# Performance work log

Measured on AMD Instinct MI355X. Metric: run time of the kernel, lower is better.

The kernel has to match this reference:

```python
import jax, jax.numpy as jnp
import numpy as np

TEMPERATURE = 8.0  # sqrt(d_k) with d_k = 64
NEG_INF = -jnp.inf


def setup_inputs() -> dict:
    key = jax.random.key(0)
    kq, kk, kv = jax.random.split(key, 3)
    b, n, d = 16, 2048, 64
    q = jax.random.normal(kq, (b, n, d), dtype=jnp.float32)
    k = jax.random.normal(kk, (b, n, d), dtype=jnp.float32)
    v = jax.random.normal(kv, (b, n, d), dtype=jnp.float32)
    # causal mask: True where attention is disallowed (strict upper triangle)
    mask = jnp.broadcast_to(jnp.triu(jnp.ones((n, n), dtype=bool), k=1), (b, n, n))
    return {"q": q, "k": k, "v": v, "mask": mask}


def reference(q, k, v, mask):
    # attn = q @ k^T / temperature   [b, n, n]
    attn = jnp.einsum('bqd,bkd->bqk', q, k) / TEMPERATURE
    attn = jnp.where(mask, NEG_INF, attn)
    attn = jax.nn.softmax(attn, axis=2)
    # output = attn @ v   [b, n, d]
    output = jnp.einsum('bqk,bkd->bqd', attn, v)
    return (output, attn)
```

## Files before the change

kernel.cpp:

```cpp
#include <hip/hip_runtime.h>


constexpr int B = 16;
constexpr int N = 2048;
constexpr int D = 64;
constexpr float INV_TEMP = 0.125f;

typedef __attribute__((ext_vector_type(8))) short bf16x8;
typedef __attribute__((ext_vector_type(4))) float f32x4;

__device__ __forceinline__ short f2bf(float f) {
    __bf16 h = (__bf16)f;
    return __builtin_bit_cast(short, h);
}

__global__ __launch_bounds__(512) void sdpa_flash(
    const float* __restrict__ q,
    const float* __restrict__ k,
    const float* __restrict__ v,
    float* __restrict__ out,
    float* __restrict__ invws)
{
    __shared__ __align__(16) short sK[64][72];
    __shared__ __align__(16) short sV[64][72];
    __shared__ __align__(16) short sPt[32][72];
    __shared__ float rsum[128];
    __shared__ float sinv[32];

    const int x = blockIdx.x;
    const int b = x >> 6;
    const int u = x & 63;
    const int rt = 63 - u;
    const int qs = rt * 32;
    const int ntiles = (rt >> 1) + 1;

    const int t    = threadIdx.x;
    const int w    = t >> 6;
    const int lane = t & 63;
    const int l15  = lane & 15;
    const int quad = lane >> 4;
    const int q8   = quad * 8;
    const int rg   = w & 1;
    const int cg   = w >> 1;

    const float* qb = q + (size_t)b * N * D;
    const float* kb = k + (size_t)b * N * D;
    const float* vb = v + (size_t)b * N * D;

    const int krow = t >> 3;
    const int kc8  = (t & 7) * 8;

    float4 kf0, kf1;
    float  vr[8];

    {
        const float4* s = (const float4*)(kb + (size_t)krow * D + kc8);
        kf0 = s[0]; kf1 = s[1];
        const float* sv = vb + (size_t)(w * 8) * D + lane;
#pragma unroll
        for (int i = 0; i < 8; ++i) vr[i] = sv[(size_t)i * D];
    }

    if (t < 256) {
        const float4* s = (const float4*)(qb + (size_t)(qs + krow) * D + kc8);
        float4 a = s[0], c4 = s[1];
        float qv[8] = {a.x,a.y,a.z,a.w, c4.x,c4.y,c4.z,c4.w};
        bf16x8 pq;
#pragma unroll
        for (int i = 0; i < 8; ++i) pq[i] = f2bf(qv[i]);
        *(bf16x8*)&sK[krow][kc8] = pq;
    }
    __syncthreads();
    const bf16x8 qa0 = *(const bf16x8*)&sK[rg * 16 + l15][q8];
    const bf16x8 qa1 = *(const bf16x8*)&sK[rg * 16 + l15][32 + q8];

    float rs[4] = {0.f, 0.f, 0.f, 0.f};
    f32x4 o = {0.f, 0.f, 0.f, 0.f};

    for (int kt = 0; kt < ntiles; ++kt) {
        __syncthreads();
        {
            float kv[8] = {kf0.x,kf0.y,kf0.z,kf0.w, kf1.x,kf1.y,kf1.z,kf1.w};
            bf16x8 pk, pv;
#pragma unroll
            for (int i = 0; i < 8; ++i) pk[i] = f2bf(kv[i]);
#pragma unroll
            for (int i = 0; i < 8; ++i) pv[i] = f2bf(vr[i]);
            *(bf16x8*)&sK[krow][kc8]  = pk;
            *(bf16x8*)&sV[lane][w*8]  = pv;
        }
        __syncthreads();
        if (kt + 1 < ntiles) {
            const float4* s = (const float4*)(kb + (size_t)((kt+1)*64 + krow) * D + kc8);
            kf0 = s[0]; kf1 = s[1];
            const float* sv = vb + (size_t)((kt+1)*64 + w*8) * D + lane;
#pragma unroll
            for (int i = 0; i < 8; ++i) vr[i] = sv[(size_t)i * D];
        }
        bf16x8 b0 = *(const bf16x8*)&sK[cg * 16 + l15][q8];
        bf16x8 b1 = *(const bf16x8*)&sK[cg * 16 + l15][32 + q8];
        f32x4 c = {0.f, 0.f, 0.f, 0.f};
        c = __builtin_amdgcn_mfma_f32_16x16x32_bf16(qa0, b0, c, 0, 0, 0);
        c = __builtin_amdgcn_mfma_f32_16x16x32_bf16(qa1, b1, c, 0, 0, 0);
        const int colg = kt * 64 + cg * 16 + l15;
#pragma unroll
        for (int r = 0; r < 4; ++r) {
            const int rowg = qs + rg * 16 + quad * 4 + r;
            float pr = (colg <= rowg) ? __expf(c[r] * INV_TEMP) : 0.f;
            rs[r] += pr;
            sPt[rg * 16 + quad * 4 + r][cg * 16 + l15] = f2bf(pr);
        }
        __syncthreads();
#pragma unroll
        for (int kc = 0; kc < 2; ++kc) {
            bf16x8 a  = *(const bf16x8*)&sPt[rg * 16 + l15][kc * 32 + q8];
            bf16x8 vf = *(const bf16x8*)&sV[cg * 16 + l15][kc * 32 + q8];
            o = __builtin_amdgcn_mfma_f32_16x16x32_bf16(a, vf, o, 0, 0, 0);
        }
    }

#pragma unroll
    for (int r = 0; r < 4; ++r) {
        float s = rs[r];
        s += __shfl_xor(s, 1);
        s += __shfl_xor(s, 2);
        s += __shfl_xor(s, 4);
        s += __shfl_xor(s, 8);
        rs[r] = s;
    }
    if (l15 == 0) {
#pragma unroll
        for (int r = 0; r < 4; ++r) rsum[w * 16 + quad * 4 + r] = rs[r];
    }
    __syncthreads();
    if (t < 32) {
        const int rg2 = t >> 4, rl = t & 15;
        float tot = rsum[(rg2 + 0) * 16 + rl] + rsum[(rg2 + 2) * 16 + rl]
                  + rsum[(rg2 + 4) * 16 + rl] + rsum[(rg2 + 6) * 16 + rl];
        sinv[t] = 1.f / tot;
        invws[(size_t)b * N + qs + t] = sinv[t];
    }
    __syncthreads();

#pragma unroll
    for (int r = 0; r < 4; ++r) {
        const int rowl = rg * 16 + quad * 4 + r;
        out[(size_t)(b * N + qs + rowl) * D + cg * 16 + l15] = o[r] * sinv[rowl];
    }
}

__global__ __launch_bounds__(512) void sdpa_attn(
    const float* __restrict__ q,
    const float* __restrict__ k,
    const float* __restrict__ attn_unused,
    float* __restrict__ attn,
    const float* __restrict__ invws)
{
    __shared__ __align__(16) short sQ[32][72];
    __shared__ float sinv[32];

    const int x = blockIdx.x;
    const int b = x >> 6;
    const int u = x & 63;
    const int rt = 63 - u;
    const int qs = rt * 32;
    const int ntiles = (rt >> 1) + 1;

    const int t    = threadIdx.x;
    const int w    = t >> 6;
    const int lane = t & 63;
    const int l15  = lane & 15;
    const int quad = lane >> 4;
    const int q8   = quad * 8;
    const int rg   = w & 1;
    const int cg   = w >> 1;

    const float* qb = q + (size_t)b * N * D;
    const float* kb = k + (size_t)b * N * D;
    float* attn_b = attn + (size_t)b * N * N;

    if (t < 256) {
        const int krow = t >> 3, kc8 = (t & 7) * 8;
        const float4* s = (const float4*)(qb + (size_t)(qs + krow) * D + kc8);
        float4 a = s[0], c4 = s[1];
        float qv[8] = {a.x,a.y,a.z,a.w, c4.x,c4.y,c4.z,c4.w};
        bf16x8 pq;
#pragma unroll
        for (int i = 0; i < 8; ++i) pq[i] = f2bf(qv[i]);
        *(bf16x8*)&sQ[krow][kc8] = pq;
    }
    if (t >= 256 && t < 288) sinv[t - 256] = invws[(size_t)b * N + qs + (t - 256)];
    __syncthreads();

    const bf16x8 qa0 = *(const bf16x8*)&sQ[rg * 16 + l15][q8];
    const bf16x8 qa1 = *(const bf16x8*)&sQ[rg * 16 + l15][32 + q8];

    const int qrow = qs + rg * 16 + l15;
    const float einv = sinv[rg * 16 + l15];
    float* arow = attn_b + (size_t)qrow * N;

    for (int kt = 0; kt < ntiles; ++kt) {
        const float* kr = kb + (size_t)(kt * 64 + cg * 16 + l15) * D;
        const float4* kp = (const float4*)(kr + q8);
        float4 k0 = kp[0], k1 = kp[1];
        const float4* kp2 = (const float4*)(kr + 32 + q8);
        float4 k2 = kp2[0], k3 = kp2[1];
        float kv[16] = {k0.x,k0.y,k0.z,k0.w, k1.x,k1.y,k1.z,k1.w,
                        k2.x,k2.y,k2.z,k2.w, k3.x,k3.y,k3.z,k3.w};
        bf16x8 kb0, kb1;
#pragma unroll
        for (int i = 0; i < 8; ++i) { kb0[i] = f2bf(kv[i]); kb1[i] = f2bf(kv[8 + i]); }

        f32x4 c = {0.f, 0.f, 0.f, 0.f};
        c = __builtin_amdgcn_mfma_f32_16x16x32_bf16(kb0, qa0, c, 0, 0, 0);
        c = __builtin_amdgcn_mfma_f32_16x16x32_bf16(kb1, qa1, c, 0, 0, 0);

        const int kg0 = kt * 64 + cg * 16 + quad * 4;
        float4 pv;
        pv.x = (kg0 + 0 <= qrow) ? __expf(c[0] * INV_TEMP) * einv : 0.f;
        pv.y = (kg0 + 1 <= qrow) ? __expf(c[1] * INV_TEMP) * einv : 0.f;
        pv.z = (kg0 + 2 <= qrow) ? __expf(c[2] * INV_TEMP) * einv : 0.f;
        pv.w = (kg0 + 3 <= qrow) ? __expf(c[3] * INV_TEMP) * einv : 0.f;
        *(float4*)(arow + kg0) = pv;
    }

    const int lim  = ntiles * 64;
    const int erow = t >> 4;
    const int ec   = (t & 15) * 4;
    float* zrow = attn_b + (size_t)(qs + erow) * N;
    const float4 z = {0.f, 0.f, 0.f, 0.f};
    for (int c0 = lim + ec; c0 < N; c0 += 64) {
        *(float4*)(zrow + c0) = z;
    }
}

extern "C" void kernel_launch(void* const* d_in, const int* in_sizes, int n_in,
                              void* d_out, int out_size, void* d_ws, size_t ws_size,
                              hipStream_t stream) {
    const float* q = (const float*)d_in[0];
    const float* k = (const float*)d_in[1];
    const float* v = (const float*)d_in[2];

    float* out  = (float*)d_out;
    float* attn = out + (size_t)B * N * D;
    float* invws = (float*)d_ws;

    sdpa_flash<<<dim3(B * 64), dim3(512), 0, stream>>>(q, k, v, out, invws);
    sdpa_attn <<<dim3(B * 64), dim3(512), 0, stream>>>(q, k, attn, attn, invws);
}
```

Before: 536.2 us.

## Fuse flash and attn-write kernels into one with paired causal row tiles

Merges the two kernels into one launch where each block handles two query row tiles, one long and one short, to balance the causal triangle's work. The normalizer stays in shared memory instead of round-tripping through a workspace buffer, and blocks are mapped so each XCD serves two batches for L2 locality. K/V shared tiles are double-buffered to drop one barrier per iteration, and K loads in the attn-write loop are prefetched one tile ahead. The grid shrinks to 512 blocks, so there is less parallelism and less latency hiding per CU.

```diff
diff --git a/kernel.cpp b/kernel.cpp
--- a/kernel.cpp
+++ b/kernel.cpp
@@ -14,25 +14,24 @@
     return __builtin_bit_cast(short, h);
 }
 
-__global__ __launch_bounds__(512) void sdpa_flash(
+__global__ __launch_bounds__(512) void sdpa_fused2(
     const float* __restrict__ q,
     const float* __restrict__ k,
     const float* __restrict__ v,
     float* __restrict__ out,
-    float* __restrict__ invws)
+    float* __restrict__ attn)
 {
-    __shared__ __align__(16) short sK[64][72];
-    __shared__ __align__(16) short sV[64][72];
+    __shared__ __align__(16) short sK[2][64][72];
+    __shared__ __align__(16) short sV[2][64][72];
     __shared__ __align__(16) short sPt[32][72];
     __shared__ float rsum[128];
     __shared__ float sinv[32];
 
-    const int x = blockIdx.x;
-    const int b = x >> 6;
-    const int u = x & 63;
-    const int rt = 63 - u;
-    const int qs = rt * 32;
-    const int ntiles = (rt >> 1) + 1;
+    const int x   = blockIdx.x;
+    const int xcd = x & 7;
+    const int idx = x >> 3;
+    const int b   = xcd * 2 + (idx & 1);
+    const int u   = idx >> 1;
 
     const int t    = threadIdx.x;
     const int w    = t >> 6;
@@ -46,191 +45,159 @@
     const float* qb = q + (size_t)b * N * D;
     const float* kb = k + (size_t)b * N * D;
     const float* vb = v + (size_t)b * N * D;
+    float* attn_b = attn + (size_t)b * N * N;
 
     const int krow = t >> 3;
     const int kc8  = (t & 7) * 8;
 
-    float4 kf0, kf1;
-    float  vr[8];
-
-    {
-        const float4* s = (const float4*)(kb + (size_t)krow * D + kc8);
-        kf0 = s[0]; kf1 = s[1];
-        const float* sv = vb + (size_t)(w * 8) * D + lane;
-#pragma unroll
-        for (int i = 0; i < 8; ++i) vr[i] = sv[(size_t)i * D];
-    }
-
-    if (t < 256) {
-        const float4* s = (const float4*)(qb + (size_t)(qs + krow) * D + kc8);
-        float4 a = s[0], c4 = s[1];
-        float qv[8] = {a.x,a.y,a.z,a.w, c4.x,c4.y,c4.z,c4.w};
-        bf16x8 pq;
-#pragma unroll
-        for (int i = 0; i < 8; ++i) pq[i] = f2bf(qv[i]);
-        *(bf16x8*)&sK[krow][kc8] = pq;
-    }
-    __syncthreads();
-    const bf16x8 qa0 = *(const bf16x8*)&sK[rg * 16 + l15][q8];
-    const bf16x8 qa1 = *(const bf16x8*)&sK[rg * 16 + l15][32 + q8];
-
-    float rs[4] = {0.f, 0.f, 0.f, 0.f};
-    f32x4 o = {0.f, 0.f, 0.f, 0.f};
-
-    for (int kt = 0; kt < ntiles; ++kt) {
-        __syncthreads();
+    for (int h = 0; h < 2; ++h) {
+        const int rt = h ? u : (63 - u);
+        const int qs = rt * 32;
+        const int nt = (rt >> 1) + 1;
+
+        float4 kf0, kf1;
+        float  vr[8];
         {
-            float kv[8] = {kf0.x,kf0.y,kf0.z,kf0.w, kf1.x,kf1.y,kf1.z,kf1.w};
-            bf16x8 pk, pv;
-#pragma unroll
-            for (int i = 0; i < 8; ++i) pk[i] = f2bf(kv[i]);
-#pragma unroll
-            for (int i = 0; i < 8; ++i) pv[i] = f2bf(vr[i]);
-            *(bf16x8*)&sK[krow][kc8]  = pk;
-            *(bf16x8*)&sV[lane][w*8]  = pv;
-        }
-        __syncthreads();
-        if (kt + 1 < ntiles) {
-            const float4* s = (const float4*)(kb + (size_t)((kt+1)*64 + krow) * D + kc8);
+            const float4* s = (const float4*)(kb + (size_t)krow * D + kc8);
             kf0 = s[0]; kf1 = s[1];
-            const float* sv = vb + (size_t)((kt+1)*64 + w*8) * D + lane;
+            const float* sv = vb + (size_t)(w * 8) * D + lane;
 #pragma unroll
             for (int i = 0; i < 8; ++i) vr[i] = sv[(size_t)i * D];
         }
-        bf16x8 b0 = *(const bf16x8*)&sK[cg * 16 + l15][q8];
-        bf16x8 b1 = *(const bf16x8*)&sK[cg * 16 + l15][32 + q8];
-        f32x4 c = {0.f, 0.f, 0.f, 0.f};
-        c = __builtin_amdgcn_mfma_f32_16x16x32_bf16(qa0, b0, c, 0, 0, 0);
-        c = __builtin_amdgcn_mfma_f32_16x16x32_bf16(qa1, b1, c, 0, 0, 0);
-        const int colg = kt * 64 + cg * 16 + l15;
+
+        __syncthreads();
+        if (t < 256) {
+            const float4* s = (const float4*)(qb + (size_t)(qs + krow) * D + kc8);
+            float4 a = s[0], c4 = s[1];
+            float qv[8] = {a.x,a.y,a.z,a.w, c4.x,c4.y,c4.z,c4.w};
+            bf16x8 pq;
+#pragma unroll
+            for (int i = 0; i < 8; ++i) pq[i] = f2bf(qv[i]);
+            *(bf16x8*)&sPt[krow][kc8] = pq;
+        }
+        __syncthreads();
+        const bf16x8 qa0 = *(const bf16x8*)&sPt[rg * 16 + l15][q8];
+        const bf16x8 qa1 = *(const bf16x8*)&sPt[rg * 16 + l15][32 + q8];
+
+        float rs[4] = {0.f, 0.f, 0.f, 0.f};
+        f32x4 o = {0.f, 0.f, 0.f, 0.f};
+
+        for (int kt = 0; kt < nt; ++kt) {
+            const int cur = kt & 1;
+            {
+                float kv[8] = {kf0.x,kf0.y,kf0.z,kf0.w, kf1.x,kf1.y,kf1.z,kf1.w};
+                bf16x8 pk, pv;
+#pragma unroll
+                for (int i = 0; i < 8; ++i) pk[i] = f2bf(kv[i]);
+#pragma unroll
+                for (int i = 0; i < 8; ++i) pv[i] = f2bf(vr[i]);
+                *(bf16x8*)&sK[cur][krow][kc8]  = pk;
+                *(bf16x8*)&sV[cur][lane][w*8]  = pv;
+            }
+            __syncthreads();
+            if (kt + 1 < nt) {
+                const float4* s = (const float4*)(kb + (size_t)((kt+1)*64 + krow) * D + kc8);
+                kf0 = s[0]; kf1 = s[1];
+                const float* sv = vb + (size_t)((kt+1)*64 + w*8) * D + lane;
+#pragma unroll
+                for (int i = 0; i < 8; ++i) vr[i] = sv[(size_t)i * D];
+            }
+            bf16x8 b0 = *(const bf16x8*)&sK[cur][cg * 16 + l15][q8];
+            bf16x8 b1 = *(const bf16x8*)&sK[cur][cg * 16 + l15][32 + q8];
+            f32x4 c = {0.f, 0.f, 0.f, 0.f};
+            c = __builtin_amdgcn_mfma_f32_16x16x32_bf16(qa0, b0, c, 0, 0, 0);
+            c = __builtin_amdgcn_mfma_f32_16x16x32_bf16(qa1, b1, c, 0, 0, 0);
+            const int colg = kt * 64 + cg * 16 + l15;
+#pragma unroll
+            for (int r = 0; r < 4; ++r) {
+                const int rowg = qs + rg * 16 + quad * 4 + r;
+                float pr = (colg <= rowg) ? __expf(c[r] * INV_TEMP) : 0.f;
+                rs[r] += pr;
+                sPt[rg * 16 + quad * 4 + r][cg * 16 + l15] = f2bf(pr);
+            }
+            __syncthreads();
+#pragma unroll
+            for (int kc = 0; kc < 2; ++kc) {
+                bf16x8 a  = *(const bf16x8*)&sPt[rg * 16 + l15][kc * 32 + q8];
+                bf16x8 vf = *(const bf16x8*)&sV[cur][cg * 16 + l15][kc * 32 + q8];
+                o = __builtin_amdgcn_mfma_f32_16x16x32_bf16(a, vf, o, 0, 0, 0);
+            }
+        }
+
 #pragma unroll
         for (int r = 0; r < 4; ++r) {
-            const int rowg = qs + rg * 16 + quad * 4 + r;
-            float pr = (colg <= rowg) ? __expf(c[r] * INV_TEMP) : 0.f;
-            rs[r] += pr;
-            sPt[rg * 16 + quad * 4 + r][cg * 16 + l15] = f2bf(pr);
-        }
-        __syncthreads();
-#pragma unroll
-        for (int kc = 0; kc < 2; ++kc) {
-            bf16x8 a  = *(const bf16x8*)&sPt[rg * 16 + l15][kc * 32 + q8];
-            bf16x8 vf = *(const bf16x8*)&sV[cg * 16 + l15][kc * 32 + q8];
-            o = __builtin_amdgcn_mfma_f32_16x16x32_bf16(a, vf, o, 0, 0, 0);
-        }
-    }
-
-#pragma unroll
-    for (int r = 0; r < 4; ++r) {
-        float s = rs[r];
-        s += __shfl_xor(s, 1);
-        s += __shfl_xor(s, 2);
-        s += __shfl_xor(s, 4);
-        s += __shfl_xor(s, 8);
-        rs[r] = s;
-    }
-    if (l15 == 0) {
-#pragma unroll
-        for (int r = 0; r < 4; ++r) rsum[w * 16 + quad * 4 + r] = rs[r];
-    }
-    __syncthreads();
-    if (t < 32) {
-        const int rg2 = t >> 4, rl = t & 15;
-        float tot = rsum[(rg2 + 0) * 16 + rl] + rsum[(rg2 + 2) * 16 + rl]
-                  + rsum[(rg2 + 4) * 16 + rl] + rsum[(rg2 + 6) * 16 + rl];
-        sinv[t] = 1.f / tot;
-        invws[(size_t)b * N + qs + t] = sinv[t];
-    }
-    __syncthreads();
-
-#pragma unroll
-    for (int r = 0; r < 4; ++r) {
-        const int rowl = rg * 16 + quad * 4 + r;
-        out[(size_t)(b * N + qs + rowl) * D + cg * 16 + l15] = o[r] * sinv[rowl];
-    }
-}
-
-__global__ __launch_bounds__(512) void sdpa_attn(
-    const float* __restrict__ q,
-    const float* __restrict__ k,
-    const float* __restrict__ attn_unused,
-    float* __restrict__ attn,
-    const float* __restrict__ invws)
-{
-    __shared__ __align__(16) short sQ[32][72];
-    __shared__ float sinv[32];
-
-    const int x = blockIdx.x;
-    const int b = x >> 6;
-    const int u = x & 63;
-    const int rt = 63 - u;
-    const int qs = rt * 32;
-    const int ntiles = (rt >> 1) + 1;
-
-    const int t    = threadIdx.x;
-    const int w    = t >> 6;
-    const int lane = t & 63;
-    const int l15  = lane & 15;
-    const int quad = lane >> 4;
-    const int q8   = quad * 8;
-    const int rg   = w & 1;
-    const int cg   = w >> 1;
-
-    const float* qb = q + (size_t)b * N * D;
-    const float* kb = k + (size_t)b * N * D;
-    float* attn_b = attn + (size_t)b * N * N;
-
-    if (t < 256) {
-        const int krow = t >> 3, kc8 = (t & 7) * 8;
-        const float4* s = (const float4*)(qb + (size_t)(qs + krow) * D + kc8);
-        float4 a = s[0], c4 = s[1];
-        float qv[8] = {a.x,a.y,a.z,a.w, c4.x,c4.y,c4.z,c4.w};
-        bf16x8 pq;
-#pragma unroll
-        for (int i = 0; i < 8; ++i) pq[i] = f2bf(qv[i]);
-        *(bf16x8*)&sQ[krow][kc8] = pq;
-    }
-    if (t >= 256 && t < 288) sinv[t - 256] = invws[(size_t)b * N + qs + (t - 256)];
-    __syncthreads();
-
-    const bf16x8 qa0 = *(const bf16x8*)&sQ[rg * 16 + l15][q8];
-    const bf16x8 qa1 = *(const bf16x8*)&sQ[rg * 16 + l15][32 + q8];
-
-    const int qrow = qs + rg * 16 + l15;
-    const float einv = sinv[rg * 16 + l15];
-    float* arow = attn_b + (size_t)qrow * N;
-
-    for (int kt = 0; kt < ntiles; ++kt) {
-        const float* kr = kb + (size_t)(kt * 64 + cg * 16 + l15) * D;
-        const float4* kp = (const float4*)(kr + q8);
-        float4 k0 = kp[0], k1 = kp[1];
-        const float4* kp2 = (const float4*)(kr + 32 + q8);
-        float4 k2 = kp2[0], k3 = kp2[1];
-        float kv[16] = {k0.x,k0.y,k0.z,k0.w, k1.x,k1.y,k1.z,k1.w,
-                        k2.x,k2.y,k2.z,k2.w, k3.x,k3.y,k3.z,k3.w};
-        bf16x8 kb0, kb1;
-#pragma unroll
-        for (int i = 0; i < 8; ++i) { kb0[i] = f2bf(kv[i]); kb1[i] = f2bf(kv[8 + i]); }
-
-        f32x4 c = {0.f, 0.f, 0.f, 0.f};
-        c = __builtin_amdgcn_mfma_f32_16x16x32_bf16(kb0, qa0, c, 0, 0, 0);
-        c = __builtin_amdgcn_mfma_f32_16x16x32_bf16(kb1, qa1, c, 0, 0, 0);
-
-        const int kg0 = kt * 64 + cg * 16 + quad * 4;
-        float4 pv;
-        pv.x = (kg0 + 0 <= qrow) ? __expf(c[0] * INV_TEMP) * einv : 0.f;
-        pv.y = (kg0 + 1 <= qrow) ? __expf(c[1] * INV_TEMP) * einv : 0.f;
-        pv.z = (kg0 + 2 <= qrow) ? __expf(c[2] * INV_TEMP) * einv : 0.f;
-        pv.w = (kg0 + 3 <= qrow) ? __expf(c[3] * INV_TEMP) * einv : 0.f;
-        *(float4*)(arow + kg0) = pv;
-    }
-
-    const int lim  = ntiles * 64;
-    const int erow = t >> 4;
-    const int ec   = (t & 15) * 4;
-    float* zrow = attn_b + (size_t)(qs + erow) * N;
-    const float4 z = {0.f, 0.f, 0.f, 0.f};
-    for (int c0 = lim + ec; c0 < N; c0 += 64) {
-        *(float4*)(zrow + c0) = z;
+            float s = rs[r];
+            s += __shfl_xor(s, 1);
+            s += __shfl_xor(s, 2);
+            s += __shfl_xor(s, 4);
+            s += __shfl_xor(s, 8);
+            rs[r] = s;
+        }
+        if (l15 == 0) {
+#pragma unroll
+            for (int r = 0; r < 4; ++r) rsum[w * 16 + quad * 4 + r] = rs[r];
+        }
+        __syncthreads();
+        if (t < 32) {
+            const int rg2 = t >> 4, rl = t & 15;
+            float tot = rsum[(rg2 + 0) * 16 + rl] + rsum[(rg2 + 2) * 16 + rl]
+                      + rsum[(rg2 + 4) * 16 + rl] + rsum[(rg2 + 6) * 16 + rl];
+            sinv[t] = 1.f / tot;
+        }
+        __syncthreads();
+
+#pragma unroll
+        for (int r = 0; r < 4; ++r) {
+            const int rowl = rg * 16 + quad * 4 + r;
+            out[(size_t)(b * N + qs + rowl) * D + cg * 16 + l15] = o[r] * sinv[rowl];
+        }
+
+        const int qrow = qs + rg * 16 + l15;
+        const float einv = sinv[rg * 16 + l15];
+        float* arow = attn_b + (size_t)qrow * N;
+
+        float4 ka0, ka1, ka2, ka3;
+        {
+            const float* kr = kb + (size_t)(cg * 16 + l15) * D;
+            const float4* kp = (const float4*)(kr + q8);
+            ka0 = kp[0]; ka1 = kp[1];
+            const float4* kp2 = (const float4*)(kr + 32 + q8);
+            ka2 = kp2[0]; ka3 = kp2[1];
+        }
+        for (int kt = 0; kt < nt; ++kt) {
+            float kv[16] = {ka0.x,ka0.y,ka0.z,ka0.w, ka1.x,ka1.y,ka1.z,ka1.w,
+                            ka2.x,ka2.y,ka2.z,ka2.w, ka3.x,ka3.y,ka3.z,ka3.w};
+            bf16x8 kb0, kb1;
+#pragma unroll
+            for (int i = 0; i < 8; ++i) { kb0[i] = f2bf(kv[i]); kb1[i] = f2bf(kv[8 + i]); }
+            if (kt + 1 < nt) {
+                const float* kr = kb + (size_t)((kt+1)*64 + cg * 16 + l15) * D;
+                const float4* kp = (const float4*)(kr + q8);
+                ka0 = kp[0]; ka1 = kp[1];
+                const float4* kp2 = (const float4*)(kr + 32 + q8);
+                ka2 = kp2[0]; ka3 = kp2[1];
+            }
+            f32x4 c = {0.f, 0.f, 0.f, 0.f};
+            c = __builtin_amdgcn_mfma_f32_16x16x32_bf16(kb0, qa0, c, 0, 0, 0);
+            c = __builtin_amdgcn_mfma_f32_16x16x32_bf16(kb1, qa1, c, 0, 0, 0);
+
+            const int kg0 = kt * 64 + cg * 16 + quad * 4;
+            float4 pv4;
+            pv4.x = (kg0 + 0 <= qrow) ? __expf(c[0] * INV_TEMP) * einv : 0.f;
+            pv4.y = (kg0 + 1 <= qrow) ? __expf(c[1] * INV_TEMP) * einv : 0.f;
+            pv4.z = (kg0 + 2 <= qrow) ? __expf(c[2] * INV_TEMP) * einv : 0.f;
+            pv4.w = (kg0 + 3 <= qrow) ? __expf(c[3] * INV_TEMP) * einv : 0.f;
+            *(float4*)(arow + kg0) = pv4;
+        }
+
+        const int lim  = nt * 64;
+        const int erow = t >> 4;
+        const int ec   = (t & 15) * 4;
+        float* zrow = attn_b + (size_t)(qs + erow) * N;
+        const float4 z = {0.f, 0.f, 0.f, 0.f};
+        for (int c0 = lim + ec; c0 < N; c0 += 64) {
+            *(float4*)(zrow + c0) = z;
+        }
     }
 }
 
@@ -243,8 +210,6 @@
 
     float* out  = (float*)d_out;
     float* attn = out + (size_t)B * N * D;
-    float* invws = (float*)d_ws;
-
-    sdpa_flash<<<dim3(B * 64), dim3(512), 0, stream>>>(q, k, v, out, invws);
-    sdpa_attn <<<dim3(B * 64), dim3(512), 0, stream>>>(q, k, attn, attn, invws);
+
+    sdpa_fused2<<<dim3(B * 32), dim3(512), 0, stream>>>(q, k, v, out, attn);
 }
```

Result: faster. 471.6 us (-12.0%).
